# Optimization experiments

Measured on AMD Instinct MI355X. Metric: run time of the kernel, lower is better.

The kernel has to match this reference:

```python
import jax, jax.numpy as jnp
import numpy as np

N = 200000   # total nodes across batched graphs
E = 800000   # directed edges (grid graph, avg degree ~4)
G = 8        # number of graphs in the batch
IN_DIM, INTER_DIM, OUT_DIM, LAYER_NUM = 2, 128, 64, 4


def setup_inputs() -> dict:
    key = jax.random.key(0)
    ks = jax.random.split(key, 10)
    x = jax.random.normal(ks[0], (N, IN_DIM), jnp.float32)
    edge_index = jax.random.randint(ks[1], (2, E), 0, N, dtype=jnp.int32)
    batch = jnp.sort(jax.random.randint(ks[2], (N,), 0, G, dtype=jnp.int32))

    def glorot(k, fan_in, fan_out):
        s = (2.0 / (fan_in + fan_out)) ** 0.5
        return jax.random.normal(k, (fan_in, fan_out), jnp.float32) * s

    W_in = glorot(ks[3], IN_DIM, INTER_DIM)
    b_in = jnp.zeros((INTER_DIM,), jnp.float32)
    W_hidden = jnp.stack([glorot(jax.random.fold_in(ks[4], i), INTER_DIM, INTER_DIM)
                          for i in range(LAYER_NUM)])
    b_hidden = jnp.zeros((LAYER_NUM, INTER_DIM), jnp.float32)
    W_out = glorot(ks[5], INTER_DIM, OUT_DIM)
    b_out = jnp.zeros((OUT_DIM,), jnp.float32)
    return {"x": x, "edge_index": edge_index, "batch": batch,
            "W_in": W_in, "b_in": b_in, "W_hidden": W_hidden,
            "b_hidden": b_hidden, "W_out": W_out, "b_out": b_out}


def reference(x, edge_index, batch, W_in, b_in, W_hidden, b_hidden, W_out, b_out):
    num_nodes = x.shape[0]
    loops = jnp.arange(num_nodes, dtype=edge_index.dtype)
    # PyG GCNConv: add self loops, symmetric degree normalization
    src = jnp.concatenate([edge_index[0], loops])
    dst = jnp.concatenate([edge_index[1], loops])
    deg = jax.ops.segment_sum(jnp.ones_like(src, x.dtype), dst, num_segments=num_nodes)
    dinv = jnp.where(deg > 0, jax.lax.rsqrt(jnp.maximum(deg, 1.0)), 0.0)
    norm = dinv[src] * dinv[dst]  # [E+N]

    def gcn_conv(h, W, b):
        m = h @ W                                  # [N, F'] dense transform
        msg = norm[:, None] * m[src]               # gather + scale
        out = jax.ops.segment_sum(msg, dst, num_segments=num_nodes)  # scatter-add
        return out + b

    h = gcn_conv(x, W_in, b_in)
    for i in range(W_hidden.shape[0]):
        h = jax.nn.relu(gcn_conv(h, W_hidden[i], b_hidden[i]))
    h = gcn_conv(h, W_out, b_out)

    # global mean pool over batch assignment, then sigmoid
    sums = jax.ops.segment_sum(h, batch, num_segments=G)
    cnts = jax.ops.segment_sum(jnp.ones((num_nodes,), h.dtype), batch, num_segments=G)
    return jax.nn.sigmoid(sums / jnp.maximum(cnts, 1.0)[:, None])
```

## Files before the change

kernel.cpp:

```cpp
#include <hip/hip_runtime.h>
#include <math.h>

#define INTER 128
#define OUTD  64
#define SCAN_T 256
#define SCAN_E 1024
#define NSLOT 64
#define NBIN  128

using bf16x8 = __attribute__((ext_vector_type(8))) short;
using f32x4  = __attribute__((ext_vector_type(4))) float;

static __device__ __forceinline__ unsigned short f2bf(float f) {
    unsigned int u = __float_as_uint(f);
    u += 0x7fffu + ((u >> 16) & 1u);
    return (unsigned short)(u >> 16);
}
static __device__ __forceinline__ unsigned int pk2(float a, float b) {
    return (unsigned int)f2bf(a) | ((unsigned int)f2bf(b) << 16);
}
static __device__ __forceinline__ float bflo(unsigned int u) { return __uint_as_float(u << 16); }
static __device__ __forceinline__ float bfhi(unsigned int u) { return __uint_as_float(u & 0xffff0000u); }

static __device__ __forceinline__ void fma8(float* a, float w, uint4 v) {
    a[0] = fmaf(w, bflo(v.x), a[0]); a[1] = fmaf(w, bfhi(v.x), a[1]);
    a[2] = fmaf(w, bflo(v.y), a[2]); a[3] = fmaf(w, bfhi(v.y), a[3]);
    a[4] = fmaf(w, bflo(v.z), a[4]); a[5] = fmaf(w, bfhi(v.z), a[5]);
    a[6] = fmaf(w, bflo(v.w), a[6]); a[7] = fmaf(w, bfhi(v.w), a[7]);
}
static __device__ __forceinline__ void seed8(float* a, float sn, uint4 v) {
    a[0] = sn * bflo(v.x); a[1] = sn * bfhi(v.x);
    a[2] = sn * bflo(v.y); a[3] = sn * bfhi(v.y);
    a[4] = sn * bflo(v.z); a[5] = sn * bfhi(v.z);
    a[6] = sn * bflo(v.w); a[7] = sn * bfhi(v.w);
}

__global__ void count_k(const int* __restrict__ dst, int* __restrict__ cnt, int E) {
    int e = blockIdx.x * 256 + threadIdx.x;
    if (e < E) atomicAdd(&cnt[dst[e]], 1);
}

__global__ void dinv_k(const int* __restrict__ cnt, float* __restrict__ dinv, int N) {
    int i = blockIdx.x * 256 + threadIdx.x;
    if (i < N) dinv[i] = rsqrtf((float)(cnt[i] + 1));
}

__global__ void scan_block(const int* __restrict__ in, int* __restrict__ out,
                           int* __restrict__ bsums, int n) {
    __shared__ int sh[SCAN_T];
    int base = blockIdx.x * SCAN_E;
    int t = threadIdx.x;
    int v[4];
    int s = 0;
#pragma unroll
    for (int i = 0; i < 4; i++) {
        int idx = base + t * 4 + i;
        v[i] = (idx < n) ? in[idx] : 0;
        s += v[i];
    }
    sh[t] = s;
    __syncthreads();
    for (int off = 1; off < SCAN_T; off <<= 1) {
        int x = (t >= off) ? sh[t - off] : 0;
        __syncthreads();
        sh[t] += x;
        __syncthreads();
    }
    int excl = (t == 0) ? 0 : sh[t - 1];
    if (bsums && t == SCAN_T - 1) bsums[blockIdx.x] = sh[t];
#pragma unroll
    for (int i = 0; i < 4; i++) {
        int idx = base + t * 4 + i;
        if (idx < n) out[idx] = excl;
        excl += v[i];
    }
}

__global__ void scan_add(int* __restrict__ out, const int* __restrict__ bsums, int n, int total) {
    int idx = blockIdx.x * SCAN_E + threadIdx.x * 4;
    int add = bsums[blockIdx.x];
#pragma unroll
    for (int i = 0; i < 4; i++) {
        int j = idx + i;
        if (j < n) out[j] += add;
    }
    if (blockIdx.x == 0 && threadIdx.x == 0) out[n] = total;
}

__global__ void scatter_k(const int* __restrict__ src, const int* __restrict__ dst,
                          const int* __restrict__ rs, int* __restrict__ cursor,
                          const float* __restrict__ dinv,
                          int2* __restrict__ cw, int E) {
    int e = blockIdx.x * 256 + threadIdx.x;
    if (e >= E) return;
    int s = src[e], d = dst[e];
    int pos = rs[d] + atomicAdd(&cursor[d], 1);
    cw[pos] = make_int2(s, __float_as_int(dinv[s] * dinv[d]));
}

__global__ __launch_bounds__(256) void dhist2_k(const int* __restrict__ cnt,
                                                int* __restrict__ blockhist,
                                                int N, int nblk) {
    __shared__ int hist[NBIN];
    int t = threadIdx.x;
    if (t < NBIN) hist[t] = 0;
    __syncthreads();
    int i = blockIdx.x * 256 + t;
    if (i < N) atomicAdd(&hist[min(cnt[i], NBIN - 1)], 1);
    __syncthreads();
    if (t < NBIN) blockhist[t * nblk + blockIdx.x] = hist[t];
}

__global__ __launch_bounds__(256) void dorder2_k(const int* __restrict__ cnt,
                                                 const int* __restrict__ offs,
                                                 int* __restrict__ order,
                                                 int N, int nblk) {
    __shared__ int cur[NBIN];
    int t = threadIdx.x;
    if (t < NBIN) cur[t] = 0;
    __syncthreads();
    int i = blockIdx.x * 256 + t;
    if (i >= N) return;
    int d = min(cnt[i], NBIN - 1);
    int r = atomicAdd(&cur[d], 1);
    order[offs[d * nblk + blockIdx.x] + r] = i;
}

__global__ void wprep_h(const float* __restrict__ W, unsigned short* __restrict__ Wt, int L) {
    int tid = blockIdx.x * 256 + threadIdx.x;
    if (tid >= L * INTER * INTER) return;
    int l = tid / (INTER * INTER);
    int r = tid % (INTER * INTER);
    int n = r / INTER, k = r % INTER;
    Wt[tid] = f2bf(W[(size_t)l * INTER * INTER + (size_t)k * INTER + n]);
}

__global__ void wprep_o(const float* __restrict__ W, unsigned short* __restrict__ Wt) {
    int tid = blockIdx.x * 256 + threadIdx.x;
    if (tid >= OUTD * INTER) return;
    int n = tid / INTER, k = tid % INTER;
    Wt[tid] = f2bf(W[(size_t)k * OUTD + n]);
}

__global__ void agg2(const float* __restrict__ x, const int* __restrict__ rs,
                     const int2* __restrict__ cw, const float* __restrict__ dinv,
                     float* __restrict__ ax, int N) {
    int i = blockIdx.x * 256 + threadIdx.x;
    if (i >= N) return;
    float di = dinv[i];
    float sn = di * di;
    float2 xv = ((const float2*)x)[i];
    float a0 = sn * xv.x, a1 = sn * xv.y;
    int e0 = rs[i], e1 = rs[i + 1];
    for (int k = e0; k < e1; k++) {
        int2 c = cw[k];
        float wk = __int_as_float(c.y);
        float2 xs = ((const float2*)x)[c.x];
        a0 += wk * xs.x;
        a1 += wk * xs.y;
    }
    ((float2*)ax)[i] = make_float2(a0, a1);
}

__global__ void gemm_in(const float* __restrict__ ax, const float* __restrict__ Wi,
                        const float* __restrict__ bi, unsigned short* __restrict__ h, int N) {
    int node = blockIdx.x * 2 + threadIdx.x / 128;
    int j = threadIdx.x % 128;
    if (node >= N) return;
    float2 a = ((const float2*)ax)[node];
    h[(size_t)node * 128 + j] = f2bf(fmaf(a.x, Wi[j], fmaf(a.y, Wi[128 + j], bi[j])));
}

__global__ __launch_bounds__(256) void fused_hidden4(
    const unsigned short* __restrict__ Hin,
    const int* __restrict__ rs, const int2* __restrict__ cw,
    const float* __restrict__ dinv, const int* __restrict__ order,
    const unsigned short* __restrict__ Wt,
    const float* __restrict__ bias,
    unsigned short* __restrict__ Hout, int N)
{
    __shared__ __align__(16) unsigned short T[32][136];
    __shared__ int nodeid[32];
    const int t = threadIdx.x;
    const int q = t & 15;
    const int gi = t >> 4;
    const int sA = blockIdx.x * 32 + gi;
    const int sB = sA + 16;
    const bool vA = sA < N, vB = sB < N;
    const int nA = vA ? order[sA] : 0;
    const int nB = vB ? order[sB] : 0;
    if (q == 0) {
        nodeid[gi]      = vA ? nA : -1;
        nodeid[gi + 16] = vB ? nB : -1;
    }

    float accA[8] = {0,0,0,0,0,0,0,0}, accB[8] = {0,0,0,0,0,0,0,0};
    if (vA) {
        float dA = dinv[nA];
        seed8(accA, dA * dA, *(const uint4*)(Hin + (size_t)nA * 128 + q * 8));
    }
    if (vB) {
        float dB = dinv[nB];
        seed8(accB, dB * dB, *(const uint4*)(Hin + (size_t)nB * 128 + q * 8));
    }
    int kA = 0, eA = 0, kB = 0, eB = 0;
    if (vA) { kA = rs[nA]; eA = rs[nA + 1]; }
    if (vB) { kB = rs[nB]; eB = rs[nB + 1]; }

    while (kA < eA || kB < eB) {
        int2 cA0 = (kA     < eA) ? cw[kA]     : make_int2(0, 0);
        int2 cA1 = (kA + 1 < eA) ? cw[kA + 1] : make_int2(0, 0);
        int2 cA2 = (kA + 2 < eA) ? cw[kA + 2] : make_int2(0, 0);
        int2 cA3 = (kA + 3 < eA) ? cw[kA + 3] : make_int2(0, 0);
        int2 cB0 = (kB     < eB) ? cw[kB]     : make_int2(0, 0);
        int2 cB1 = (kB + 1 < eB) ? cw[kB + 1] : make_int2(0, 0);
        int2 cB2 = (kB + 2 < eB) ? cw[kB + 2] : make_int2(0, 0);
        int2 cB3 = (kB + 3 < eB) ? cw[kB + 3] : make_int2(0, 0);
        uint4 vA0 = *(const uint4*)(Hin + (size_t)cA0.x * 128 + q * 8);
        uint4 vA1 = *(const uint4*)(Hin + (size_t)cA1.x * 128 + q * 8);
        uint4 vA2 = *(const uint4*)(Hin + (size_t)cA2.x * 128 + q * 8);
        uint4 vA3 = *(const uint4*)(Hin + (size_t)cA3.x * 128 + q * 8);
        uint4 vB0 = *(const uint4*)(Hin + (size_t)cB0.x * 128 + q * 8);
        uint4 vB1 = *(const uint4*)(Hin + (size_t)cB1.x * 128 + q * 8);
        uint4 vB2 = *(const uint4*)(Hin + (size_t)cB2.x * 128 + q * 8);
        uint4 vB3 = *(const uint4*)(Hin + (size_t)cB3.x * 128 + q * 8);
        fma8(accA, __int_as_float(cA0.y), vA0);
        fma8(accA, __int_as_float(cA1.y), vA1);
        fma8(accA, __int_as_float(cA2.y), vA2);
        fma8(accA, __int_as_float(cA3.y), vA3);
        fma8(accB, __int_as_float(cB0.y), vB0);
        fma8(accB, __int_as_float(cB1.y), vB1);
        fma8(accB, __int_as_float(cB2.y), vB2);
        fma8(accB, __int_as_float(cB3.y), vB3);
        kA += 4; kB += 4;
    }

    {
        uint4 oA = make_uint4(pk2(accA[0], accA[1]), pk2(accA[2], accA[3]),
                              pk2(accA[4], accA[5]), pk2(accA[6], accA[7]));
        uint4 oB = make_uint4(pk2(accB[0], accB[1]), pk2(accB[2], accB[3]),
                              pk2(accB[4], accB[5]), pk2(accB[6], accB[7]));
        *(uint4*)&T[gi][q * 8] = oA;
        *(uint4*)&T[gi + 16][q * 8] = oB;
    }
    __syncthreads();

    const int wv = t >> 6;
    const int lane = t & 63;
    const int r15 = lane & 15;
    const int kg = lane >> 4;

    bf16x8 bfr[2][4];
#pragma unroll
    for (int nc = 0; nc < 2; nc++)
#pragma unroll
        for (int ks = 0; ks < 4; ks++)
            bfr[nc][ks] = *(const bf16x8*)&T[nc * 16 + r15][kg * 8 + ks * 32];

    f32x4 acc[2][2];
#pragma unroll
    for (int nc = 0; nc < 2; nc++)
#pragma unroll
        for (int c = 0; c < 2; c++) acc[nc][c] = (f32x4){0.f, 0.f, 0.f, 0.f};

#pragma unroll
    for (int c = 0; c < 2; c++) {
        const unsigned short* wrow = Wt + (size_t)(wv * 32 + c * 16 + r15) * 128 + kg * 8;
#pragma unroll
        for (int ks = 0; ks < 4; ks++) {
            bf16x8 afr = *(const bf16x8*)(wrow + ks * 32);
            acc[0][c] = __builtin_amdgcn_mfma_f32_16x16x32_bf16(afr, bfr[0][ks], acc[0][c], 0, 0, 0);
            acc[1][c] = __builtin_amdgcn_mfma_f32_16x16x32_bf16(afr, bfr[1][ks], acc[1][c], 0, 0, 0);
        }
    }

#pragma unroll
    for (int nc = 0; nc < 2; nc++) {
        const int node = nodeid[nc * 16 + r15];
        if (node >= 0) {
#pragma unroll
            for (int c = 0; c < 2; c++) {
                int col = wv * 32 + c * 16 + kg * 4;
                float4 bv = *(const float4*)(bias + col);
                float v0 = fmaxf(acc[nc][c][0] + bv.x, 0.f);
                float v1 = fmaxf(acc[nc][c][1] + bv.y, 0.f);
                float v2 = fmaxf(acc[nc][c][2] + bv.z, 0.f);
                float v3 = fmaxf(acc[nc][c][3] + bv.w, 0.f);
                *(uint2*)(Hout + (size_t)node * 128 + col) = make_uint2(pk2(v0, v1), pk2(v2, v3));
            }
        }
    }
}

__global__ __launch_bounds__(256) void gemm_out(const unsigned short* __restrict__ Hin,
                                                const unsigned short* __restrict__ Wt,
                                                unsigned short* __restrict__ g, int N) {
    const int wv = threadIdx.x >> 6;
    const int lane = threadIdx.x & 63;
    const int r15 = lane & 15;
    const int kg = lane >> 4;
    const int node0 = blockIdx.x * 64 + wv * 16;
    if (node0 >= N) return;

    int arow = node0 + r15;
    if (arow >= N) arow = N - 1;
    bf16x8 bfr[4];
#pragma unroll
    for (int ks = 0; ks < 4; ks++)
        bfr[ks] = __builtin_nontemporal_load(
            (const bf16x8*)(Hin + (size_t)arow * 128 + kg * 8 + ks * 32));

    f32x4 acc[4];
#pragma unroll
    for (int c = 0; c < 4; c++) acc[c] = (f32x4){0.f, 0.f, 0.f, 0.f};

#pragma unroll
    for (int c = 0; c < 4; c++) {
        const unsigned short* wrow = Wt + (size_t)(c * 16 + r15) * 128 + kg * 8;
#pragma unroll
        for (int ks = 0; ks < 4; ks++) {
            bf16x8 afr = *(const bf16x8*)(wrow + ks * 32);
            acc[c] = __builtin_amdgcn_mfma_f32_16x16x32_bf16(afr, bfr[ks], acc[c], 0, 0, 0);
        }
    }
    const int node = node0 + r15;
    if (node < N) {
#pragma unroll
        for (int c = 0; c < 4; c++) {
            int col = c * 16 + kg * 4;
            *(uint2*)(g + (size_t)node * 64 + col) =
                make_uint2(pk2(acc[c][0], acc[c][1]), pk2(acc[c][2], acc[c][3]));
        }
    }
}

__global__ __launch_bounds__(256) void fused_last2(
    const unsigned short* __restrict__ g,
    const int* __restrict__ rs, const int2* __restrict__ cw,
    const float* __restrict__ dinv, const int* __restrict__ batch,
    float* __restrict__ gsum , int N)
{
    __shared__ __align__(16) float R[64][68];
    __shared__ int gid[64];
    const int t = threadIdx.x;
    const int q = t & 7;
    const int gi = t >> 3;
    const int nA = blockIdx.x * 64 + gi;
    const int nB = nA + 32;
    const bool vA = nA < N, vB = nB < N;

    float accA[8] = {0,0,0,0,0,0,0,0}, accB[8] = {0,0,0,0,0,0,0,0};
    if (vA) {
        float dA = dinv[nA];
        seed8(accA, dA * dA, *(const uint4*)(g + (size_t)nA * 64 + q * 8));
    }
    if (vB) {
        float dB = dinv[nB];
        seed8(accB, dB * dB, *(const uint4*)(g + (size_t)nB * 64 + q * 8));
    }
    int kA = 0, eA = 0, kB = 0, eB = 0;
    if (vA) { kA = rs[nA]; eA = rs[nA + 1]; }
    if (vB) { kB = rs[nB]; eB = rs[nB + 1]; }

    while (kA < eA || kB < eB) {
        int2 cA0 = (kA     < eA) ? cw[kA]     : make_int2(0, 0);
        int2 cA1 = (kA + 1 < eA) ? cw[kA + 1] : make_int2(0, 0);
        int2 cA2 = (kA + 2 < eA) ? cw[kA + 2] : make_int2(0, 0);
        int2 cA3 = (kA + 3 < eA) ? cw[kA + 3] : make_int2(0, 0);
        int2 cB0 = (kB     < eB) ? cw[kB]     : make_int2(0, 0);
        int2 cB1 = (kB + 1 < eB) ? cw[kB + 1] : make_int2(0, 0);
        int2 cB2 = (kB + 2 < eB) ? cw[kB + 2] : make_int2(0, 0);
        int2 cB3 = (kB + 3 < eB) ? cw[kB + 3] : make_int2(0, 0);
        uint4 vA0 = *(const uint4*)(g + (size_t)cA0.x * 64 + q * 8);
        uint4 vA1 = *(const uint4*)(g + (size_t)cA1.x * 64 + q * 8);
        uint4 vA2 = *(const uint4*)(g + (size_t)cA2.x * 64 + q * 8);
        uint4 vA3 = *(const uint4*)(g + (size_t)cA3.x * 64 + q * 8);
        uint4 vB0 = *(const uint4*)(g + (size_t)cB0.x * 64 + q * 8);
        uint4 vB1 = *(const uint4*)(g + (size_t)cB1.x * 64 + q * 8);
        uint4 vB2 = *(const uint4*)(g + (size_t)cB2.x * 64 + q * 8);
        uint4 vB3 = *(const uint4*)(g + (size_t)cB3.x * 64 + q * 8);
        fma8(accA, __int_as_float(cA0.y), vA0);
        fma8(accA, __int_as_float(cA1.y), vA1);
        fma8(accA, __int_as_float(cA2.y), vA2);
        fma8(accA, __int_as_float(cA3.y), vA3);
        fma8(accB, __int_as_float(cB0.y), vB0);
        fma8(accB, __int_as_float(cB1.y), vB1);
        fma8(accB, __int_as_float(cB2.y), vB2);
        fma8(accB, __int_as_float(cB3.y), vB3);
        kA += 4; kB += 4;
    }

#pragma unroll
    for (int j = 0; j < 8; j += 4) {
        *(float4*)&R[gi][q * 8 + j]      = make_float4(accA[j], accA[j+1], accA[j+2], accA[j+3]);
        *(float4*)&R[gi + 32][q * 8 + j] = make_float4(accB[j], accB[j+1], accB[j+2], accB[j+3]);
    }
    if (q == 0) {
        gid[gi]      = vA ? batch[nA] : -1;
        gid[gi + 32] = vB ? batch[nB] : -1;
    }
    __syncthreads();

    const int f = t & 63;
    const int half = t >> 6;
    const int slot = blockIdx.x & (NSLOT - 1);
    float acc = 0.f;
    int cur = -1;
    for (int r = 0; r < 16; r++) {
        int row = half * 16 + r;
        int gg = gid[row];
        if (gg != cur) {
            if (cur >= 0) atomicAdd(&gsum[(size_t)(slot * 8 + cur) * 64 + f], acc);
            acc = 0.f; cur = gg;
        }
        if (gg >= 0) acc += R[row][f];
    }
    if (cur >= 0) atomicAdd(&gsum[(size_t)(slot * 8 + cur) * 64 + f], acc);
}

__global__ void gbound_k(const int* __restrict__ batch, int* __restrict__ gstart, int N, int G) {
    int i = blockIdx.x * 256 + threadIdx.x;
    if (i >= N) return;
    int b = batch[i];
    int prev = (i == 0) ? -1 : batch[i - 1];
    for (int g = prev + 1; g <= b; g++) gstart[g] = i;
    if (i == N - 1) for (int g = b + 1; g <= G; g++) gstart[g] = N;
}

__global__ void final4_k(const float* __restrict__ gsum, const int* __restrict__ gstart,
                         const float* __restrict__ b_out, float* __restrict__ out) {
    int t = threadIdx.x;
    int g = t >> 6, f = t & 63;
    float s = 0.f;
    for (int sl = 0; sl < NSLOT; sl++) s += gsum[(size_t)(sl * 8 + g) * 64 + f];
    int c = gstart[g + 1] - gstart[g];
    float v = s / (float)max(c, 1) + b_out[f];
    out[g * 64 + f] = 1.f / (1.f + expf(-v));
}

extern "C" void kernel_launch(void* const* d_in, const int* in_sizes, int n_in,
                              void* d_out, int out_size, void* d_ws, size_t ws_size,
                              hipStream_t stream) {
    const float* x     = (const float*)d_in[0];
    const int*   ei    = (const int*)d_in[1];
    const int*   batch = (const int*)d_in[2];
    const float* W_in  = (const float*)d_in[3];
    const float* b_in  = (const float*)d_in[4];
    const float* W_h   = (const float*)d_in[5];
    const float* b_h   = (const float*)d_in[6];
    const float* W_out = (const float*)d_in[7];
    const float* b_out = (const float*)d_in[8];

    const int N = in_sizes[2];
    const int E = in_sizes[1] / 2;
    const int L = in_sizes[5] / (INTER * INTER);
    const int G = 8;
    const int* src = ei;
    const int* dst = ei + E;
    const int nblk = (N + 255) / 256;
    const int nbh = NBIN * nblk;

    char* ws = (char*)d_ws;
    size_t off = 0;
    auto alloc = [&](size_t bytes) -> void* {
        void* p = ws + off;
        off += (bytes + 255) & ~(size_t)255;
        return p;
    };
    int*   cnt    = (int*)alloc((size_t)N * 4);
    int*   cursor = (int*)alloc((size_t)N * 4);
    int*   rs     = (int*)alloc((size_t)(N + 1) * 4);
    int*   bsums  = (int*)alloc(4096);
    float* dinv   = (float*)alloc((size_t)N * 4);
    int2*  cw     = (int2*)alloc((size_t)E * 8);
    float* ax     = (float*)alloc((size_t)N * 2 * 4);
    unsigned short* h   = (unsigned short*)alloc((size_t)N * INTER * 2);
    unsigned short* h2  = (unsigned short*)alloc((size_t)N * INTER * 2);
    unsigned short* g   = (unsigned short*)alloc((size_t)N * OUTD * 2);
    unsigned short* Wht = (unsigned short*)alloc((size_t)L * INTER * INTER * 2);
    unsigned short* Wot = (unsigned short*)alloc((size_t)OUTD * INTER * 2);
    float* gsum   = (float*)alloc((size_t)NSLOT * 8 * OUTD * 4);
    int*   gstart = (int*)alloc((G + 1) * 4);
    int*   bh     = (int*)alloc((size_t)(nbh + 1) * 4);
    int*   order  = (int*)alloc((size_t)N * 4);
    (void)ws_size; (void)n_in;

    hipMemsetAsync(cnt, 0, (size_t)N * 4, stream);
    hipMemsetAsync(cursor, 0, (size_t)N * 4, stream);
    hipMemsetAsync(gsum, 0, (size_t)NSLOT * 8 * OUTD * 4, stream);

    count_k<<<(E + 255) / 256, 256, 0, stream>>>(dst, cnt, E);
    dinv_k<<<nblk, 256, 0, stream>>>(cnt, dinv, N);
    int nsb = (N + SCAN_E - 1) / SCAN_E;
    scan_block<<<nsb, SCAN_T, 0, stream>>>(cnt, rs, bsums, N);
    scan_block<<<1, SCAN_T, 0, stream>>>(bsums, bsums, nullptr, nsb);
    scan_add<<<nsb, SCAN_T, 0, stream>>>(rs, bsums, N, E);
    scatter_k<<<(E + 255) / 256, 256, 0, stream>>>(src, dst, rs, cursor, dinv, cw, E);
    gbound_k<<<nblk, 256, 0, stream>>>(batch, gstart, N, G);

    dhist2_k<<<nblk, 256, 0, stream>>>(cnt, bh, N, nblk);
    int nsb2 = (nbh + SCAN_E - 1) / SCAN_E;
    scan_block<<<nsb2, SCAN_T, 0, stream>>>(bh, bh, bsums, nbh);
    scan_block<<<1, SCAN_T, 0, stream>>>(bsums, bsums, nullptr, nsb2);
    scan_add<<<nsb2, SCAN_T, 0, stream>>>(bh, bsums, nbh, N);
    dorder2_k<<<nblk, 256, 0, stream>>>(cnt, bh, order, N, nblk);

    wprep_h<<<(L * INTER * INTER + 255) / 256, 256, 0, stream>>>(W_h, Wht, L);
    wprep_o<<<(OUTD * INTER + 255) / 256, 256, 0, stream>>>(W_out, Wot);

    agg2<<<nblk, 256, 0, stream>>>(x, rs, cw, dinv, ax, N);
    gemm_in<<<(N + 1) / 2, 256, 0, stream>>>(ax, W_in, b_in, h, N);

    unsigned short* hin = h;
    unsigned short* hout = h2;
    for (int l = 0; l < L; l++) {
        fused_hidden4<<<(N + 31) / 32, 256, 0, stream>>>(
            hin, rs, cw, dinv, order, Wht + (size_t)l * INTER * INTER, b_h + (size_t)l * INTER, hout, N);
        unsigned short* tmp = hin; hin = hout; hout = tmp;
    }

    gemm_out<<<(N + 63) / 64, 256, 0, stream>>>(hin, Wot, g, N);
    fused_last2<<<(N + 63) / 64, 256, 0, stream>>>(g, rs, cw, dinv, batch, gsum, N);
    final4_k<<<1, 512, 0, stream>>>(gsum, gstart, b_out, (float*)d_out);
}
```

Measured before the change: 542.9 us.

## Process 64 nodes per block in fused hidden layer with weight-stationary MFMA

Each block of the fused hidden-layer kernel now aggregates 64 destination nodes instead of 32, with each 16-lane group interleaving four neighbour lists. That puts up to 16 independent row gathers in flight per iteration. The GEMM stage now loads the weight fragments once per wave and reuses them across four 16-node column tiles, halving weight reloads per node. In exchange it uses more registers and shared memory, which may reduce occupancy, and the shared while loop runs until the longest of four neighbour lists finishes, which adds divergence.

```diff
diff --git a/kernel.cpp b/kernel.cpp
--- a/kernel.cpp
+++ b/kernel.cpp
@@ -171,7 +171,7 @@
     h[(size_t)node * 128 + j] = f2bf(fmaf(a.x, Wi[j], fmaf(a.y, Wi[128 + j], bi[j])));
 }
 
-__global__ __launch_bounds__(256) void fused_hidden4(
+__global__ __launch_bounds__(256) void fused_hidden5(
     const unsigned short* __restrict__ Hin,
     const int* __restrict__ rs, const int2* __restrict__ cw,
     const float* __restrict__ dinv, const int* __restrict__ order,
@@ -179,69 +179,58 @@
     const float* __restrict__ bias,
     unsigned short* __restrict__ Hout, int N)
 {
-    __shared__ __align__(16) unsigned short T[32][136];
-    __shared__ int nodeid[32];
+    __shared__ __align__(16) unsigned short T[64][136];
+    __shared__ int nodeid[64];
     const int t = threadIdx.x;
     const int q = t & 15;
     const int gi = t >> 4;
-    const int sA = blockIdx.x * 32 + gi;
-    const int sB = sA + 16;
-    const bool vA = sA < N, vB = sB < N;
-    const int nA = vA ? order[sA] : 0;
-    const int nB = vB ? order[sB] : 0;
-    if (q == 0) {
-        nodeid[gi]      = vA ? nA : -1;
-        nodeid[gi + 16] = vB ? nB : -1;
-    }
-
-    float accA[8] = {0,0,0,0,0,0,0,0}, accB[8] = {0,0,0,0,0,0,0,0};
-    if (vA) {
-        float dA = dinv[nA];
-        seed8(accA, dA * dA, *(const uint4*)(Hin + (size_t)nA * 128 + q * 8));
-    }
-    if (vB) {
-        float dB = dinv[nB];
-        seed8(accB, dB * dB, *(const uint4*)(Hin + (size_t)nB * 128 + q * 8));
-    }
-    int kA = 0, eA = 0, kB = 0, eB = 0;
-    if (vA) { kA = rs[nA]; eA = rs[nA + 1]; }
-    if (vB) { kB = rs[nB]; eB = rs[nB + 1]; }
-
-    while (kA < eA || kB < eB) {
-        int2 cA0 = (kA     < eA) ? cw[kA]     : make_int2(0, 0);
-        int2 cA1 = (kA + 1 < eA) ? cw[kA + 1] : make_int2(0, 0);
-        int2 cA2 = (kA + 2 < eA) ? cw[kA + 2] : make_int2(0, 0);
-        int2 cA3 = (kA + 3 < eA) ? cw[kA + 3] : make_int2(0, 0);
-        int2 cB0 = (kB     < eB) ? cw[kB]     : make_int2(0, 0);
-        int2 cB1 = (kB + 1 < eB) ? cw[kB + 1] : make_int2(0, 0);
-        int2 cB2 = (kB + 2 < eB) ? cw[kB + 2] : make_int2(0, 0);
-        int2 cB3 = (kB + 3 < eB) ? cw[kB + 3] : make_int2(0, 0);
-        uint4 vA0 = *(const uint4*)(Hin + (size_t)cA0.x * 128 + q * 8);
-        uint4 vA1 = *(const uint4*)(Hin + (size_t)cA1.x * 128 + q * 8);
-        uint4 vA2 = *(const uint4*)(Hin + (size_t)cA2.x * 128 + q * 8);
-        uint4 vA3 = *(const uint4*)(Hin + (size_t)cA3.x * 128 + q * 8);
-        uint4 vB0 = *(const uint4*)(Hin + (size_t)cB0.x * 128 + q * 8);
-        uint4 vB1 = *(const uint4*)(Hin + (size_t)cB1.x * 128 + q * 8);
-        uint4 vB2 = *(const uint4*)(Hin + (size_t)cB2.x * 128 + q * 8);
-        uint4 vB3 = *(const uint4*)(Hin + (size_t)cB3.x * 128 + q * 8);
-        fma8(accA, __int_as_float(cA0.y), vA0);
-        fma8(accA, __int_as_float(cA1.y), vA1);
-        fma8(accA, __int_as_float(cA2.y), vA2);
-        fma8(accA, __int_as_float(cA3.y), vA3);
-        fma8(accB, __int_as_float(cB0.y), vB0);
-        fma8(accB, __int_as_float(cB1.y), vB1);
-        fma8(accB, __int_as_float(cB2.y), vB2);
-        fma8(accB, __int_as_float(cB3.y), vB3);
-        kA += 4; kB += 4;
-    }
-
-    {
-        uint4 oA = make_uint4(pk2(accA[0], accA[1]), pk2(accA[2], accA[3]),
-                              pk2(accA[4], accA[5]), pk2(accA[6], accA[7]));
-        uint4 oB = make_uint4(pk2(accB[0], accB[1]), pk2(accB[2], accB[3]),
-                              pk2(accB[4], accB[5]), pk2(accB[6], accB[7]));
-        *(uint4*)&T[gi][q * 8] = oA;
-        *(uint4*)&T[gi + 16][q * 8] = oB;
+
+    float ac[4][8];
+    int kk[4], ee[4];
+#pragma unroll
+    for (int j = 0; j < 4; j++) {
+        int s = blockIdx.x * 64 + j * 16 + gi;
+        bool v = s < N;
+        int n = v ? order[s] : -1;
+        if (q == 0) nodeid[j * 16 + gi] = n;
+        if (v) {
+            float d = dinv[n];
+            seed8(ac[j], d * d, *(const uint4*)(Hin + (size_t)n * 128 + q * 8));
+            kk[j] = rs[n]; ee[j] = rs[n + 1];
+        } else {
+#pragma unroll
+            for (int x2 = 0; x2 < 8; x2++) ac[j][x2] = 0.f;
+            kk[j] = 0; ee[j] = 0;
+        }
+    }
+
+    while (kk[0] < ee[0] || kk[1] < ee[1] || kk[2] < ee[2] || kk[3] < ee[3]) {
+        int2 c[4][4];
+#pragma unroll
+        for (int j = 0; j < 4; j++)
+#pragma unroll
+            for (int u = 0; u < 4; u++)
+                c[j][u] = (kk[j] + u < ee[j]) ? cw[kk[j] + u] : make_int2(0, 0);
+        uint4 v[4][4];
+#pragma unroll
+        for (int j = 0; j < 4; j++)
+#pragma unroll
+            for (int u = 0; u < 4; u++)
+                v[j][u] = *(const uint4*)(Hin + (size_t)c[j][u].x * 128 + q * 8);
+#pragma unroll
+        for (int j = 0; j < 4; j++) {
+#pragma unroll
+            for (int u = 0; u < 4; u++)
+                fma8(ac[j], __int_as_float(c[j][u].y), v[j][u]);
+            kk[j] += 4;
+        }
+    }
+
+#pragma unroll
+    for (int j = 0; j < 4; j++) {
+        *(uint4*)&T[j * 16 + gi][q * 8] =
+            make_uint4(pk2(ac[j][0], ac[j][1]), pk2(ac[j][2], ac[j][3]),
+                       pk2(ac[j][4], ac[j][5]), pk2(ac[j][6], ac[j][7]));
     }
     __syncthreads();
 
@@ -250,42 +239,41 @@
     const int r15 = lane & 15;
     const int kg = lane >> 4;
 
-    bf16x8 bfr[2][4];
-#pragma unroll
-    for (int nc = 0; nc < 2; nc++)
+    bf16x8 wfr[2][4];
+#pragma unroll
+    for (int c2 = 0; c2 < 2; c2++) {
+        const unsigned short* wrow = Wt + (size_t)(wv * 32 + c2 * 16 + r15) * 128 + kg * 8;
 #pragma unroll
         for (int ks = 0; ks < 4; ks++)
-            bfr[nc][ks] = *(const bf16x8*)&T[nc * 16 + r15][kg * 8 + ks * 32];
-
-    f32x4 acc[2][2];
-#pragma unroll
-    for (int nc = 0; nc < 2; nc++)
-#pragma unroll
-        for (int c = 0; c < 2; c++) acc[nc][c] = (f32x4){0.f, 0.f, 0.f, 0.f};
-
-#pragma unroll
-    for (int c = 0; c < 2; c++) {
-        const unsigned short* wrow = Wt + (size_t)(wv * 32 + c * 16 + r15) * 128 + kg * 8;
-#pragma unroll
-        for (int ks = 0; ks < 4; ks++) {
-            bf16x8 afr = *(const bf16x8*)(wrow + ks * 32);
-            acc[0][c] = __builtin_amdgcn_mfma_f32_16x16x32_bf16(afr, bfr[0][ks], acc[0][c], 0, 0, 0);
-            acc[1][c] = __builtin_amdgcn_mfma_f32_16x16x32_bf16(afr, bfr[1][ks], acc[1][c], 0, 0, 0);
-        }
-    }
-
-#pragma unroll
-    for (int nc = 0; nc < 2; nc++) {
+            wfr[c2][ks] = *(const bf16x8*)(wrow + ks * 32);
+    }
+
+#pragma unroll
+    for (int nc = 0; nc < 4; nc++) {
+        bf16x8 bfr[4];
+#pragma unroll
+        for (int ks = 0; ks < 4; ks++)
+            bfr[ks] = *(const bf16x8*)&T[nc * 16 + r15][kg * 8 + ks * 32];
+
+        f32x4 acc[2];
+        acc[0] = (f32x4){0.f, 0.f, 0.f, 0.f};
+        acc[1] = (f32x4){0.f, 0.f, 0.f, 0.f};
+#pragma unroll
+        for (int c2 = 0; c2 < 2; c2++)
+#pragma unroll
+            for (int ks = 0; ks < 4; ks++)
+                acc[c2] = __builtin_amdgcn_mfma_f32_16x16x32_bf16(wfr[c2][ks], bfr[ks], acc[c2], 0, 0, 0);
+
         const int node = nodeid[nc * 16 + r15];
         if (node >= 0) {
 #pragma unroll
-            for (int c = 0; c < 2; c++) {
-                int col = wv * 32 + c * 16 + kg * 4;
+            for (int c2 = 0; c2 < 2; c2++) {
+                int col = wv * 32 + c2 * 16 + kg * 4;
                 float4 bv = *(const float4*)(bias + col);
-                float v0 = fmaxf(acc[nc][c][0] + bv.x, 0.f);
-                float v1 = fmaxf(acc[nc][c][1] + bv.y, 0.f);
-                float v2 = fmaxf(acc[nc][c][2] + bv.z, 0.f);
-                float v3 = fmaxf(acc[nc][c][3] + bv.w, 0.f);
+                float v0 = fmaxf(acc[c2][0] + bv.x, 0.f);
+                float v1 = fmaxf(acc[c2][1] + bv.y, 0.f);
+                float v2 = fmaxf(acc[c2][2] + bv.z, 0.f);
+                float v3 = fmaxf(acc[c2][3] + bv.w, 0.f);
                 *(uint2*)(Hout + (size_t)node * 128 + col) = make_uint2(pk2(v0, v1), pk2(v2, v3));
             }
         }
@@ -514,7 +502,7 @@
     unsigned short* hin = h;
     unsigned short* hout = h2;
     for (int l = 0; l < L; l++) {
-        fused_hidden4<<<(N + 31) / 32, 256, 0, stream>>>(
+        fused_hidden5<<<(N + 63) / 64, 256, 0, stream>>>(
             hin, rs, cw, dinv, order, Wht + (size_t)l * INTER * INTER, b_h + (size_t)l * INTER, hout, N);
         unsigned short* tmp = hin; hin = hout; hout = tmp;
     }
```

Result: slower. 581.8 us (+7.2%).
